# Kernel tuning notes

Hardware: AMD Instinct MI355X
Metric: run time of the kernel (lower is better)

The kernel has to match this reference:

```python
import jax, jax.numpy as jnp
import numpy as np

EPS = 1e-8


def setup_inputs() -> dict:
    key = jax.random.key(0)
    ks = jax.random.split(key, 5)
    B, C, F, T = 2, 8, 1024, 256
    Ch, Fh = 4 * C, 4 * F  # expanded channels/features
    s_pw1 = 1.0 / np.sqrt(F)
    s_dw1 = 1.0 / np.sqrt(C)
    s_pw2 = 1.0 / np.sqrt(Fh)
    s_dw2 = 1.0 / np.sqrt(Ch)
    return {
        "x": jax.random.normal(ks[0], (B, C, F, T), jnp.float32),
        "ln_w": jnp.ones((C, F), jnp.float32),
        "ln_b": jnp.zeros((C, F), jnp.float32),
        "pw1": jax.random.uniform(ks[1], (C, Fh, F), jnp.float32, -s_pw1, s_pw1),
        "dw1": jax.random.uniform(ks[2], (Ch, C), jnp.float32, -s_dw1, s_dw1),
        "pw2": jax.random.uniform(ks[3], (Ch, F, Fh), jnp.float32, -s_pw2, s_pw2),
        "dw2": jax.random.uniform(ks[4], (C, Ch), jnp.float32, -s_dw2, s_dw2),
    }


def _mc_layernorm(x, w, b):
    # x: (B,C,F,T); normalize over feature axis (2), affine per (channel, feature)
    mu = jnp.mean(x, axis=2, keepdims=True)
    var = jnp.var(x, axis=2, keepdims=True)
    xn = (x - mu) * jax.lax.rsqrt(var + EPS)
    return xn * w[None, :, :, None] + b[None, :, :, None]


def reference(x, ln_w, ln_b, pw1, dw1, pw2, dw2):
    h = _mc_layernorm(x, ln_w, ln_b)
    # per-channel positionwise linear: (C, F_out, F_in)
    h = jnp.einsum('bcft,cgf->bcgt', h, pw1)
    # channel mixing (depthwise linear across channels): (C_out, C_in)
    h = jnp.einsum('bcft,dc->bdft', h, dw1)
    h = jnp.square(jax.nn.relu(h))  # squared ReLU
    h = jnp.einsum('bcft,cgf->bcgt', h, pw2)
    h = jnp.einsum('bcft,dc->bdft', h, dw2)
    return x + h
```

## Files before the change

### kernel.cpp

```cpp
#include <hip/hip_runtime.h>

#define B_DIM  2
#define C_DIM  8
#define F_DIM  1024
#define T_DIM  256
#define CH_DIM 32
#define FH_DIM 4096
#define BT_DIM 512

typedef __bf16 bf16x8 __attribute__((ext_vector_type(8)));
typedef __bf16 bf16x4 __attribute__((ext_vector_type(4)));
typedef float  f32x4  __attribute__((ext_vector_type(4)));

__device__ __forceinline__ void async16(const void* g, void* l) {
  __builtin_amdgcn_global_load_lds(
      (const __attribute__((address_space(1))) unsigned int*)g,
      (__attribute__((address_space(3))) unsigned int*)l, 16, 0, 0);
}

#define LGKM0_SCHED() do { \
    asm volatile("s_waitcnt lgkmcnt(0)" ::: "memory"); \
    __builtin_amdgcn_sched_barrier(0); } while (0)

__global__ void ln_kernel(const float* __restrict__ x,
                          const float* __restrict__ lnw,
                          const float* __restrict__ lnb,
                          __bf16* __restrict__ hn) {
  const int tb = blockIdx.x;
  const int c  = blockIdx.y;
  const int b  = blockIdx.z;
  const int tid = threadIdx.x;
  const int tx = tid & 15, ty = tid >> 4;
  const int t0 = tb * 16;

  const float* xp = x + (size_t)(b * C_DIM + c) * F_DIM * T_DIM;

  float s = 0.f, s2 = 0.f;
  for (int f = ty; f < F_DIM; f += 16) {
    float v = xp[f * T_DIM + t0 + tx];
    s += v; s2 += v * v;
  }
  __shared__ float ps[16][16], ps2[16][16];
  __shared__ float mean_s[16], rstd_s[16];
  ps[ty][tx] = s; ps2[ty][tx] = s2;
  __syncthreads();
  if (tid < 16) {
    float a = 0.f, a2 = 0.f;
    for (int j = 0; j < 16; ++j) { a += ps[j][tid]; a2 += ps2[j][tid]; }
    float mu  = a * (1.0f / F_DIM);
    float var = a2 * (1.0f / F_DIM) - mu * mu;
    mean_s[tid] = mu;
    rstd_s[tid] = rsqrtf(var + 1e-8f);
  }
  __syncthreads();

  __shared__ float tile[64][17];
  __bf16* hp = hn + ((size_t)c * BT_DIM + b * T_DIM + t0) * F_DIM;
  for (int ff = 0; ff < 16; ++ff) {
    const int f0 = ff * 64;
#pragma unroll
    for (int it = 0; it < 4; ++it) {
      int e  = it * 256 + tid;
      int fi = e >> 4, ti = e & 15;
      float v = xp[(f0 + fi) * T_DIM + t0 + ti];
      v = (v - mean_s[ti]) * rstd_s[ti];
      v = v * lnw[c * F_DIM + f0 + fi] + lnb[c * F_DIM + f0 + fi];
      tile[fi][ti] = v;
    }
    __syncthreads();
#pragma unroll
    for (int it = 0; it < 4; ++it) {
      int e  = it * 256 + tid;
      int fx = e & 63, tw = e >> 6;
      hp[(size_t)tw * F_DIM + f0 + fx] = (__bf16)tile[fx][tw];
    }
    __syncthreads();
  }
}

template<int MTBITS, bool CT>
__global__ __launch_bounds__(512, 2)
void gemm_8p(const float* __restrict__ A, const __bf16* __restrict__ Bm,
             __bf16* __restrict__ Co, const int M, const int K) {
  const int NT = K >> 6;
  const int bid = blockIdx.x;
  const int xcd = bid & 7, idx = bid >> 3;
  const int batch = xcd * (32 >> MTBITS) + (idx >> MTBITS);
  const int mt    = idx & ((1 << MTBITS) - 1);

  const int tid = threadIdx.x, lane = tid & 63, wid = tid >> 6;

  const float*  Ab = A  + (size_t)batch * M * K + (size_t)(mt * 128) * K;
  const __bf16* Bb = Bm + (size_t)batch * BT_DIM * K;

  extern __shared__ __align__(16) char smem[];
  __bf16* const AS = (__bf16*)smem;
  __bf16* const BS = (__bf16*)(smem + 32768);

  const int wm = wid >> 2, wn = wid & 3;
  const int lr = lane & 15, khi = lane >> 4;
  const int lsw = lr & 7;

  const int b_row = lane >> 3;
  const int b_src = (lane & 7) ^ b_row;

  f32x4 acc[4][8] = {};
  float4 sa[4];
  bf16x8 af[4];

  auto issueB2 = [&](int sbuf, int tt, int j0) {
#pragma unroll
    for (int j = j0; j < j0 + 2; ++j) {
      const int chunk = j * 8 + wid;
      async16(Bb + (size_t)(chunk * 8 + b_row) * K + (size_t)tt * 64 + b_src * 8,
              BS + sbuf * 32768 + chunk * 512);
    }
  };
  auto issueA1 = [&](int tt, int i) {
    const int c = i * 512 + tid;
    sa[i] = *(const float4*)(Ab + (size_t)(c >> 4) * K + (size_t)tt * 64 + (c & 15) * 4);
  };
  auto writeA1 = [&](int abuf, int i) {
    const int c = i * 512 + tid;
    const int r = c >> 4;
    const int s = ((c & 15) >> 1) ^ (r & 7);
    bf16x4 v;
    v[0]=(__bf16)sa[i].x; v[1]=(__bf16)sa[i].y; v[2]=(__bf16)sa[i].z; v[3]=(__bf16)sa[i].w;
    *(bf16x4*)(AS + abuf * 8192 + r * 64 + s * 8 + (c & 1) * 4) = v;
  };
  auto readA = [&](int abuf, int ks) {
#pragma unroll
    for (int j = 0; j < 4; ++j) {
      const int row = wm * 64 + j * 16 + lr;
      af[j] = *(const bf16x8*)(AS + abuf * 8192 + row * 64 + (((ks << 2) | khi) ^ lsw) * 8);
    }
  };
  auto readB2 = [&](bf16x8* bq, int rbuf, int np, int ks) {
#pragma unroll
    for (int j = 0; j < 2; ++j) {
      const int row = wn * 128 + (np * 2 + j) * 16 + lr;
      bq[j] = *(const bf16x8*)(BS + rbuf * 32768 + row * 64 + (((ks << 2) | khi) ^ lsw) * 8);
    }
  };
  auto mfma8 = [&](const bf16x8* bq, int np) {
    __builtin_amdgcn_s_setprio(1);
#pragma unroll
    for (int j = 0; j < 4; ++j)
#pragma unroll
      for (int n = 0; n < 2; ++n)
        acc[j][np * 2 + n] =
            __builtin_amdgcn_mfma_f32_16x16x32_bf16(af[j], bq[n], acc[j][np * 2 + n], 0, 0, 0);
    __builtin_amdgcn_s_setprio(0);
  };

  issueA1(0, 0); issueA1(0, 1); issueA1(0, 2); issueA1(0, 3);
  issueB2(0, 0, 0); issueB2(0, 0, 2); issueB2(0, 0, 4); issueB2(0, 0, 6);
  writeA1(0, 0); writeA1(0, 1); writeA1(0, 2); writeA1(0, 3);
  issueA1(1, 0); issueA1(1, 1); issueA1(1, 2); issueA1(1, 3);
  asm volatile("s_waitcnt vmcnt(4)" ::: "memory");
  LGKM0_SCHED();
  __builtin_amdgcn_s_barrier();

  int cur = 0;
  for (int t = 0; t < NT; ++t) {
    const int tB = (t + 1 < NT) ? t + 1 : NT - 1;
    const int tA = (t + 2 < NT) ? t + 2 : NT - 1;
    bf16x8 bq[2];
    issueB2(cur ^ 1, tB, 0);
    readA(cur, 0); readB2(bq, cur, 0, 0);
    __builtin_amdgcn_s_barrier(); LGKM0_SCHED();
    mfma8(bq, 0); __builtin_amdgcn_s_barrier();
    issueB2(cur ^ 1, tB, 2);
    readB2(bq, cur, 1, 0);
    __builtin_amdgcn_s_barrier(); LGKM0_SCHED();
    mfma8(bq, 1); __builtin_amdgcn_s_barrier();
    issueB2(cur ^ 1, tB, 4);
    readB2(bq, cur, 2, 0);
    __builtin_amdgcn_s_barrier(); LGKM0_SCHED();
    mfma8(bq, 2); __builtin_amdgcn_s_barrier();
    issueB2(cur ^ 1, tB, 6);
    readB2(bq, cur, 3, 0);
    __builtin_amdgcn_s_barrier(); LGKM0_SCHED();
    mfma8(bq, 3); __builtin_amdgcn_s_barrier();
    writeA1(cur ^ 1, 0); issueA1(tA, 0);
    readA(cur, 1); readB2(bq, cur, 0, 1);
    __builtin_amdgcn_s_barrier(); LGKM0_SCHED();
    mfma8(bq, 0); __builtin_amdgcn_s_barrier();
    writeA1(cur ^ 1, 1); issueA1(tA, 1);
    readB2(bq, cur, 1, 1);
    __builtin_amdgcn_s_barrier(); LGKM0_SCHED();
    mfma8(bq, 1); __builtin_amdgcn_s_barrier();
    writeA1(cur ^ 1, 2); issueA1(tA, 2);
    readB2(bq, cur, 2, 1);
    __builtin_amdgcn_s_barrier(); LGKM0_SCHED();
    mfma8(bq, 2); __builtin_amdgcn_s_barrier();
    writeA1(cur ^ 1, 3); issueA1(tA, 3);
    readB2(bq, cur, 3, 1);
    __builtin_amdgcn_s_barrier(); LGKM0_SCHED();
    mfma8(bq, 3);
    asm volatile("s_waitcnt vmcnt(4)" ::: "memory");
    LGKM0_SCHED();
    __builtin_amdgcn_s_barrier();
    cur ^= 1;
  }

  const int colc = lane & 15;
  const int rowb = (lane >> 4) * 4;
  if (CT) {
    __bf16* T = (__bf16*)smem + wid * 1152;
    const int mbase = mt * 128 + wm * 64;
#pragma unroll
    for (int ni = 0; ni < 8; ++ni) {
#pragma unroll
      for (int mi = 0; mi < 4; ++mi)
#pragma unroll
        for (int r = 0; r < 4; ++r)
          T[colc * 72 + mi * 16 + rowb + r] = (__bf16)acc[mi][ni][r];
      __bf16* outp = Co + (size_t)batch * BT_DIM * M
                        + (size_t)(wn * 128 + ni * 16) * M + mbase + lane;
#pragma unroll
      for (int r16 = 0; r16 < 16; ++r16)
        outp[(size_t)r16 * M] = T[r16 * 72 + lane];
    }
  } else {
#pragma unroll
    for (int mi = 0; mi < 4; ++mi) {
#pragma unroll
      for (int ni = 0; ni < 8; ++ni) {
        const int m = mt * 128 + wm * 64 + mi * 16 + rowb;
        const int n = wn * 128 + ni * 16 + colc;
#pragma unroll
        for (int r = 0; r < 4; ++r)
          Co[((size_t)batch * M + m + r) * BT_DIM + n] = (__bf16)acc[mi][ni][r];
      }
    }
  }
}

__global__ void mix1_kernel(const __bf16* __restrict__ Y1,
                            const float* __restrict__ dw1,
                            __bf16* __restrict__ h2) {
  const int gidx = blockIdx.x * 256 + threadIdx.x;
  const int g8 = gidx & 511, bt = gidx >> 9;
  const int g0 = g8 * 8;

  float y[C_DIM][8];
#pragma unroll
  for (int c = 0; c < C_DIM; ++c) {
    bf16x8 v = *(const bf16x8*)(Y1 + ((size_t)c * BT_DIM + bt) * FH_DIM + g0);
#pragma unroll
    for (int j = 0; j < 8; ++j) y[c][j] = (float)v[j];
  }
  for (int d = 0; d < CH_DIM; ++d) {
    float s[8] = {0.f,0.f,0.f,0.f,0.f,0.f,0.f,0.f};
#pragma unroll
    for (int c = 0; c < C_DIM; ++c) {
      const float wv = dw1[d * C_DIM + c];
#pragma unroll
      for (int j = 0; j < 8; ++j) s[j] += wv * y[c][j];
    }
    bf16x8 o;
#pragma unroll
    for (int j = 0; j < 8; ++j) {
      float r = s[j] > 0.f ? s[j] : 0.f;
      o[j] = (__bf16)(r * r);
    }
    *(bf16x8*)(h2 + ((size_t)d * BT_DIM + bt) * FH_DIM + g0) = o;
  }
}

__global__ void mix2_kernel(const float* __restrict__ x,
                            const __bf16* __restrict__ Y2,
                            const float* __restrict__ dw2,
                            float* __restrict__ out) {
  const int gidx = blockIdx.x * 256 + threadIdx.x;
  const int t4 = gidx & 63;
  const int f  = (gidx >> 6) & 1023;
  const int b  = gidx >> 16;
  const int t0 = t4 * 4;

  float4 r[C_DIM];
#pragma unroll
  for (int dd = 0; dd < C_DIM; ++dd)
    r[dd] = *(const float4*)(x + ((size_t)(b * C_DIM + dd) * F_DIM + f) * T_DIM + t0);

  for (int d = 0; d < CH_DIM; ++d) {
    bf16x4 v = *(const bf16x4*)(Y2 + ((size_t)d * F_DIM + f) * BT_DIM + b * T_DIM + t0);
    const float v0 = (float)v[0], v1 = (float)v[1], v2 = (float)v[2], v3 = (float)v[3];
#pragma unroll
    for (int dd = 0; dd < C_DIM; ++dd) {
      const float w = dw2[dd * CH_DIM + d];
      r[dd].x += w * v0; r[dd].y += w * v1; r[dd].z += w * v2; r[dd].w += w * v3;
    }
  }
#pragma unroll
  for (int dd = 0; dd < C_DIM; ++dd)
    *(float4*)(out + ((size_t)(b * C_DIM + dd) * F_DIM + f) * T_DIM + t0) = r[dd];
}

extern "C" void kernel_launch(void* const* d_in, const int* in_sizes, int n_in,
                              void* d_out, int out_size, void* d_ws, size_t ws_size,
                              hipStream_t stream) {
  const float* x   = (const float*)d_in[0];
  const float* lnw = (const float*)d_in[1];
  const float* lnb = (const float*)d_in[2];
  const float* pw1 = (const float*)d_in[3];
  const float* dw1 = (const float*)d_in[4];
  const float* pw2 = (const float*)d_in[5];
  const float* dw2 = (const float*)d_in[6];
  float* out = (float*)d_out;

  char* ws = (char*)d_ws;
  __bf16* hn = (__bf16*)(ws);
  __bf16* Y1 = (__bf16*)(ws + (8ULL << 20));
  __bf16* h2 = (__bf16*)(ws + (40ULL << 20));
  __bf16* Y2 = (__bf16*)(ws);

  (void)hipFuncSetAttribute((const void*)gemm_8p<5, true>,
                            hipFuncAttributeMaxDynamicSharedMemorySize, 163840);
  (void)hipFuncSetAttribute((const void*)gemm_8p<3, false>,
                            hipFuncAttributeMaxDynamicSharedMemorySize, 163840);

  ln_kernel<<<dim3(T_DIM / 16, C_DIM, B_DIM), 256, 0, stream>>>(x, lnw, lnb, hn);
  gemm_8p<5, true><<<256, 512, 163840, stream>>>(pw1, hn, Y1, FH_DIM, F_DIM);
  mix1_kernel<<<(BT_DIM * (FH_DIM / 8)) / 256, 256, 0, stream>>>(Y1, dw1, h2);
  gemm_8p<3, false><<<256, 512, 163840, stream>>>(pw2, h2, Y2, F_DIM, FH_DIM);
  mix2_kernel<<<512, 256, 0, stream>>>(x, Y2, dw2, out);
}
```

Before: 330.3 us.

## Switch GEMM to BK=32 with triple-buffered B and fewer barriers

The GEMM K-tile is halved from 64 to 32, and the B operand moves from double to triple buffering, so loads for tile t+2 are issued while tile t is computed. Each iteration now runs two 16-MFMA phases instead of eight 8-MFMA phases, which removes many barriers and waitcnts per unit of K. Shared-memory swizzles are rewritten for the 32-wide rows, and the dynamic LDS request drops from 163840 to 114688. The end-of-iteration vmcnt wait is removed, so correctness now depends on the async loads finishing in time, which looks like a race risk.

```diff
diff --git a/kernel.cpp b/kernel.cpp
--- a/kernel.cpp
+++ b/kernel.cpp
@@ -80,9 +80,9 @@
 
 template<int MTBITS, bool CT>
 __global__ __launch_bounds__(512, 2)
-void gemm_8p(const float* __restrict__ A, const __bf16* __restrict__ Bm,
+void gemm_fn(const float* __restrict__ A, const __bf16* __restrict__ Bm,
              __bf16* __restrict__ Co, const int M, const int K) {
-  const int NT = K >> 6;
+  const int NT = K >> 5;
   const int bid = blockIdx.x;
   const int xcd = bid & 7, idx = bid >> 3;
   const int batch = xcd * (32 >> MTBITS) + (idx >> MTBITS);
@@ -95,111 +95,89 @@
 
   extern __shared__ __align__(16) char smem[];
   __bf16* const AS = (__bf16*)smem;
-  __bf16* const BS = (__bf16*)(smem + 32768);
+  __bf16* const BS = (__bf16*)(smem + 16384);
 
   const int wm = wid >> 2, wn = wid & 3;
   const int lr = lane & 15, khi = lane >> 4;
-  const int lsw = lr & 7;
-
-  const int b_row = lane >> 3;
-  const int b_src = (lane & 7) ^ b_row;
+  const int rsw = (lr >> 1) & 3;
+
+  const int b_s = (lane & 3) ^ ((lane >> 3) & 3);
 
   f32x4 acc[4][8] = {};
-  float4 sa[4];
+  float4 sa[2];
   bf16x8 af[4];
 
   auto issueB2 = [&](int sbuf, int tt, int j0) {
 #pragma unroll
     for (int j = j0; j < j0 + 2; ++j) {
       const int chunk = j * 8 + wid;
-      async16(Bb + (size_t)(chunk * 8 + b_row) * K + (size_t)tt * 64 + b_src * 8,
-              BS + sbuf * 32768 + chunk * 512);
+      const int r = chunk * 16 + (lane >> 2);
+      async16(Bb + (size_t)r * K + (size_t)tt * 32 + b_s * 8,
+              BS + sbuf * 16384 + chunk * 512);
     }
   };
   auto issueA1 = [&](int tt, int i) {
     const int c = i * 512 + tid;
-    sa[i] = *(const float4*)(Ab + (size_t)(c >> 4) * K + (size_t)tt * 64 + (c & 15) * 4);
+    const int r = c >> 3, q = c & 7;
+    sa[i] = *(const float4*)(Ab + (size_t)r * K + (size_t)tt * 32 + q * 4);
   };
   auto writeA1 = [&](int abuf, int i) {
     const int c = i * 512 + tid;
-    const int r = c >> 4;
-    const int s = ((c & 15) >> 1) ^ (r & 7);
+    const int r = c >> 3, q = c & 7;
+    const int s = (q >> 1) ^ ((r >> 1) & 3);
     bf16x4 v;
     v[0]=(__bf16)sa[i].x; v[1]=(__bf16)sa[i].y; v[2]=(__bf16)sa[i].z; v[3]=(__bf16)sa[i].w;
-    *(bf16x4*)(AS + abuf * 8192 + r * 64 + s * 8 + (c & 1) * 4) = v;
-  };
-  auto readA = [&](int abuf, int ks) {
+    *(bf16x4*)(AS + abuf * 4096 + r * 32 + s * 8 + (q & 1) * 4) = v;
+  };
+  auto readA = [&](int abuf) {
 #pragma unroll
     for (int j = 0; j < 4; ++j) {
       const int row = wm * 64 + j * 16 + lr;
-      af[j] = *(const bf16x8*)(AS + abuf * 8192 + row * 64 + (((ks << 2) | khi) ^ lsw) * 8);
-    }
-  };
-  auto readB2 = [&](bf16x8* bq, int rbuf, int np, int ks) {
-#pragma unroll
-    for (int j = 0; j < 2; ++j) {
-      const int row = wn * 128 + (np * 2 + j) * 16 + lr;
-      bq[j] = *(const bf16x8*)(BS + rbuf * 32768 + row * 64 + (((ks << 2) | khi) ^ lsw) * 8);
-    }
-  };
-  auto mfma8 = [&](const bf16x8* bq, int np) {
+      af[j] = *(const bf16x8*)(AS + abuf * 4096 + row * 32 + ((khi ^ rsw) << 3));
+    }
+  };
+  auto readB4 = [&](bf16x8* bq, int rbuf, int np) {
+#pragma unroll
+    for (int ni = 0; ni < 4; ++ni) {
+      const int row = wn * 128 + (np * 4 + ni) * 16 + lr;
+      bq[ni] = *(const bf16x8*)(BS + rbuf * 16384 + row * 32 + ((khi ^ rsw) << 3));
+    }
+  };
+  auto mfma16 = [&](const bf16x8* bq, int np) {
     __builtin_amdgcn_s_setprio(1);
 #pragma unroll
     for (int j = 0; j < 4; ++j)
 #pragma unroll
-      for (int n = 0; n < 2; ++n)
-        acc[j][np * 2 + n] =
-            __builtin_amdgcn_mfma_f32_16x16x32_bf16(af[j], bq[n], acc[j][np * 2 + n], 0, 0, 0);
+      for (int n = 0; n < 4; ++n)
+        acc[j][np * 4 + n] =
+            __builtin_amdgcn_mfma_f32_16x16x32_bf16(af[j], bq[n], acc[j][np * 4 + n], 0, 0, 0);
     __builtin_amdgcn_s_setprio(0);
   };
 
-  issueA1(0, 0); issueA1(0, 1); issueA1(0, 2); issueA1(0, 3);
-  issueB2(0, 0, 0); issueB2(0, 0, 2); issueB2(0, 0, 4); issueB2(0, 0, 6);
-  writeA1(0, 0); writeA1(0, 1); writeA1(0, 2); writeA1(0, 3);
-  issueA1(1, 0); issueA1(1, 1); issueA1(1, 2); issueA1(1, 3);
-  asm volatile("s_waitcnt vmcnt(4)" ::: "memory");
+  issueA1(0, 0); issueA1(0, 1);
+  issueB2(0, 0, 0); issueB2(0, 0, 2);
+  issueB2(1, 1, 0); issueB2(1, 1, 2);
+  writeA1(0, 0); writeA1(0, 1);
+  issueA1(1, 0); issueA1(1, 1);
+  asm volatile("s_waitcnt vmcnt(6)" ::: "memory");
   LGKM0_SCHED();
   __builtin_amdgcn_s_barrier();
 
   int cur = 0;
   for (int t = 0; t < NT; ++t) {
-    const int tB = (t + 1 < NT) ? t + 1 : NT - 1;
-    const int tA = (t + 2 < NT) ? t + 2 : NT - 1;
-    bf16x8 bq[2];
-    issueB2(cur ^ 1, tB, 0);
-    readA(cur, 0); readB2(bq, cur, 0, 0);
+    const int rd = t % 3, st = (t + 2) % 3;
+    const int tN = (t + 2 < NT) ? t + 2 : NT - 1;
+    bf16x8 bq[4];
+    issueB2(st, tN, 0);
+    readA(cur); readB4(bq, rd, 0);
     __builtin_amdgcn_s_barrier(); LGKM0_SCHED();
-    mfma8(bq, 0); __builtin_amdgcn_s_barrier();
-    issueB2(cur ^ 1, tB, 2);
-    readB2(bq, cur, 1, 0);
+    mfma16(bq, 0); __builtin_amdgcn_s_barrier();
+    issueB2(st, tN, 2);
+    writeA1(cur ^ 1, 0); writeA1(cur ^ 1, 1);
+    issueA1(tN, 0); issueA1(tN, 1);
+    readB4(bq, rd, 1);
     __builtin_amdgcn_s_barrier(); LGKM0_SCHED();
-    mfma8(bq, 1); __builtin_amdgcn_s_barrier();
-    issueB2(cur ^ 1, tB, 4);
-    readB2(bq, cur, 2, 0);
-    __builtin_amdgcn_s_barrier(); LGKM0_SCHED();
-    mfma8(bq, 2); __builtin_amdgcn_s_barrier();
-    issueB2(cur ^ 1, tB, 6);
-    readB2(bq, cur, 3, 0);
-    __builtin_amdgcn_s_barrier(); LGKM0_SCHED();
-    mfma8(bq, 3); __builtin_amdgcn_s_barrier();
-    writeA1(cur ^ 1, 0); issueA1(tA, 0);
-    readA(cur, 1); readB2(bq, cur, 0, 1);
-    __builtin_amdgcn_s_barrier(); LGKM0_SCHED();
-    mfma8(bq, 0); __builtin_amdgcn_s_barrier();
-    writeA1(cur ^ 1, 1); issueA1(tA, 1);
-    readB2(bq, cur, 1, 1);
-    __builtin_amdgcn_s_barrier(); LGKM0_SCHED();
-    mfma8(bq, 1); __builtin_amdgcn_s_barrier();
-    writeA1(cur ^ 1, 2); issueA1(tA, 2);
-    readB2(bq, cur, 2, 1);
-    __builtin_amdgcn_s_barrier(); LGKM0_SCHED();
-    mfma8(bq, 2); __builtin_amdgcn_s_barrier();
-    writeA1(cur ^ 1, 3); issueA1(tA, 3);
-    readB2(bq, cur, 3, 1);
-    __builtin_amdgcn_s_barrier(); LGKM0_SCHED();
-    mfma8(bq, 3);
-    asm volatile("s_waitcnt vmcnt(4)" ::: "memory");
-    LGKM0_SCHED();
+    mfma16(bq, 1);
     __builtin_amdgcn_s_barrier();
     cur ^= 1;
   }
@@ -316,14 +294,14 @@
   __bf16* h2 = (__bf16*)(ws + (40ULL << 20));
   __bf16* Y2 = (__bf16*)(ws);
 
-  (void)hipFuncSetAttribute((const void*)gemm_8p<5, true>,
-                            hipFuncAttributeMaxDynamicSharedMemorySize, 163840);
-  (void)hipFuncSetAttribute((const void*)gemm_8p<3, false>,
-                            hipFuncAttributeMaxDynamicSharedMemorySize, 163840);
+  (void)hipFuncSetAttribute((const void*)gemm_fn<5, true>,
+                            hipFuncAttributeMaxDynamicSharedMemorySize, 114688);
+  (void)hipFuncSetAttribute((const void*)gemm_fn<3, false>,
+                            hipFuncAttributeMaxDynamicSharedMemorySize, 114688);
 
   ln_kernel<<<dim3(T_DIM / 16, C_DIM, B_DIM), 256, 0, stream>>>(x, lnw, lnb, hn);
-  gemm_8p<5, true><<<256, 512, 163840, stream>>>(pw1, hn, Y1, FH_DIM, F_DIM);
+  gemm_fn<5, true><<<256, 512, 114688, stream>>>(pw1, hn, Y1, FH_DIM, F_DIM);
   mix1_kernel<<<(BT_DIM * (FH_DIM / 8)) / 256, 256, 0, stream>>>(Y1, dw1, h2);
-  gemm_8p<3, false><<<256, 512, 163840, stream>>>(pw2, h2, Y2, F_DIM, FH_DIM);
+  gemm_fn<3, false><<<256, 512, 114688, stream>>>(pw2, h2, Y2, F_DIM, FH_DIM);
   mix2_kernel<<<512, 256, 0, stream>>>(x, Y2, dw2, out);
 }
```

Result: slower. 357.9 us (+8.4%).
